# Kernel optimization log

Measured on AMD Instinct MI355X. Metric: run time of the kernel, lower is better.

Reference implementation:

```python
import jax, jax.numpy as jnp
import numpy as np

NEG = -9e15
ALPHA = 0.2  # LeakyReLU negative slope


def setup_inputs() -> dict:
    key = jax.random.key(0)
    k1, k2, k3, k4, k5, k6 = jax.random.split(key, 6)
    N, Fin, Fout = 8192, 512, 64
    x = jax.random.normal(k1, (N, Fin), dtype=jnp.float32)
    adj = jax.random.randint(k2, (N, N), 0, 2, dtype=jnp.int32)
    W = jax.random.normal(k3, (Fin, Fout), dtype=jnp.float32) * 0.05
    b = jax.random.normal(k4, (Fout,), dtype=jnp.float32) * 0.05
    a = jax.random.normal(k5, (2 * Fout,), dtype=jnp.float32) * 0.05
    a_b = jax.random.normal(k6, (), dtype=jnp.float32) * 0.05
    return {"x": x, "adj": adj, "W": W, "b": b, "a": a, "a_b": a_b}


def reference(x, adj, W, b, a, a_b):
    Fout = W.shape[1]
    h = x @ W + b  # [N, Fout]
    # attn([h_i, h_j]) decomposes: e[i,j] = h_i . a_src + h_j . a_dst + a_b
    # (avoids materializing the [N, N, 2F] concat tensor; same math)
    s_src = h @ a[:Fout]  # [N]
    s_dst = h @ a[Fout:]  # [N]
    energy = s_src[:, None] + s_dst[None, :] + a_b  # [N, N]
    energy = jnp.where(energy > 0, energy, ALPHA * energy)  # LeakyReLU
    masked = jnp.where(adj > 0, energy, NEG)
    attn = jax.nn.softmax(masked, axis=-1)  # dropout p=0 in eval
    h_prime = attn @ h  # [N, Fout]
    return jax.nn.elu(h_prime)  # concat=True path
```

## Files before the change

kernel.cpp:

```cpp
#include <hip/hip_runtime.h>
#include <hip/hip_bf16.h>

#define N_NODES 8192
#define FIN 512
#define FOUT 64
#define LRELU_ALPHA 0.2f

typedef __attribute__((ext_vector_type(8))) short short8;
typedef __attribute__((ext_vector_type(4))) float floatx4;

static __device__ __forceinline__ short f2bf_bits(float x) {
    union { __hip_bfloat16 b; short s; } u; u.b = __float2bfloat16(x); return u.s;
}

__global__ __launch_bounds__(256) void adj_bits(
    const int* __restrict__ adj, unsigned long long* __restrict__ bits)
{
    const int lane = threadIdx.x & 63;
    const int wid = blockIdx.x * 4 + (threadIdx.x >> 6);
    const size_t base = (size_t)wid * 128;
    const int* src = adj + base * 64 + lane;
    #pragma unroll 8
    for (int t = 0; t < 128; ++t) {
        int v = src[t * 64];
        unsigned long long m = __ballot(v > 0);
        if (lane == 0) bits[base + t] = m;
    }
}

#define GH_KT 128
__global__ __launch_bounds__(256) void gat_h(
    const float* __restrict__ x, const float* __restrict__ W,
    const float* __restrict__ bias, const float* __restrict__ a,
    const float* __restrict__ a_b,
    float* __restrict__ s_src, float* __restrict__ s_dst,
    unsigned short* __restrict__ hswz)
{
    __shared__ __align__(16) float xlds[2][16][GH_KT];

    const int lane = threadIdx.x & 63;
    const int wave = threadIdx.x >> 6;
    const int i0 = blockIdx.x * 16;
    const int r0 = i0 + wave * 4;

    auto stage = [&](int buf, int k0) {
        #pragma unroll
        for (int d = 0; d < 2; ++d) {
            const int row = wave * 4 + d * 2 + (lane >> 5);
            const float* g = x + (size_t)(i0 + row) * FIN + k0 + (lane & 31) * 4;
            __builtin_amdgcn_global_load_lds(
                (const __attribute__((address_space(1))) float*)g,
                (__attribute__((address_space(3))) float*)&xlds[buf][wave * 4 + d * 2][0],
                16, 0, 0);
        }
    };

    float acc0 = 0.f, acc1 = 0.f, acc2 = 0.f, acc3 = 0.f;

    stage(0, 0);
    for (int kt = 0; kt < FIN / GH_KT; ++kt) {
        asm volatile("s_waitcnt vmcnt(0)" ::: "memory");
        __builtin_amdgcn_sched_barrier(0);
        if (kt + 1 < FIN / GH_KT) stage((kt + 1) & 1, (kt + 1) * GH_KT);

        const float* xt = &xlds[kt & 1][wave * 4][0];
        const int k0 = kt * GH_KT;
        #pragma unroll 4
        for (int k4 = 0; k4 < GH_KT / 4; ++k4) {
            float w0 = W[(k0 + k4 * 4 + 0) * FOUT + lane];
            float w1 = W[(k0 + k4 * 4 + 1) * FOUT + lane];
            float w2 = W[(k0 + k4 * 4 + 2) * FOUT + lane];
            float w3 = W[(k0 + k4 * 4 + 3) * FOUT + lane];
            float4 xa = *reinterpret_cast<const float4*>(xt + 0 * GH_KT + k4 * 4);
            float4 xb = *reinterpret_cast<const float4*>(xt + 1 * GH_KT + k4 * 4);
            float4 xc = *reinterpret_cast<const float4*>(xt + 2 * GH_KT + k4 * 4);
            float4 xd = *reinterpret_cast<const float4*>(xt + 3 * GH_KT + k4 * 4);
            acc0 = fmaf(xa.w, w3, fmaf(xa.z, w2, fmaf(xa.y, w1, fmaf(xa.x, w0, acc0))));
            acc1 = fmaf(xb.w, w3, fmaf(xb.z, w2, fmaf(xb.y, w1, fmaf(xb.x, w0, acc1))));
            acc2 = fmaf(xc.w, w3, fmaf(xc.z, w2, fmaf(xc.y, w1, fmaf(xc.x, w0, acc2))));
            acc3 = fmaf(xd.w, w3, fmaf(xd.z, w2, fmaf(xd.y, w1, fmaf(xd.x, w0, acc3))));
        }
    }

    float bb = bias[lane];
    acc0 += bb; acc1 += bb; acc2 += bb; acc3 += bb;

    {
        const int ks = r0 >> 5;
        const int n = lane >> 4;
        const int lane_dst = (lane & 15) + (((r0 >> 3) & 3) << 4);
        const int e0 = r0 & 7;
        ushort4 pk;
        pk.x = (unsigned short)f2bf_bits(acc0);
        pk.y = (unsigned short)f2bf_bits(acc1);
        pk.z = (unsigned short)f2bf_bits(acc2);
        pk.w = (unsigned short)f2bf_bits(acc3);
        *reinterpret_cast<ushort4*>(
            hswz + (size_t)((ks * 4 + n) * 64 + lane_dst) * 8 + e0) = pk;
    }

    float asrc = a[lane], adst = a[FOUT + lane];
    float ab = a_b[0];
    float ss0 = acc0 * asrc, ss1 = acc1 * asrc, ss2 = acc2 * asrc, ss3 = acc3 * asrc;
    float sd0 = acc0 * adst, sd1 = acc1 * adst, sd2 = acc2 * adst, sd3 = acc3 * adst;
    #pragma unroll
    for (int m = 32; m >= 1; m >>= 1) {
        ss0 += __shfl_xor(ss0, m); ss1 += __shfl_xor(ss1, m);
        ss2 += __shfl_xor(ss2, m); ss3 += __shfl_xor(ss3, m);
        sd0 += __shfl_xor(sd0, m); sd1 += __shfl_xor(sd1, m);
        sd2 += __shfl_xor(sd2, m); sd3 += __shfl_xor(sd3, m);
    }
    if (lane == 0) {
        float4 vs = { ss0 + ab, ss1 + ab, ss2 + ab, ss3 + ab };
        float4 vd = { sd0, sd1, sd2, sd3 };
        *reinterpret_cast<float4*>(s_src + r0) = vs;
        *reinterpret_cast<float4*>(s_dst + r0) = vd;
    }
}

__global__ __launch_bounds__(512) void gat_attn(
    const unsigned int* __restrict__ bits,
    const float* __restrict__ s_src,
    const float* __restrict__ s_dst,
    const unsigned short* __restrict__ hswz,
    float* __restrict__ out)
{
    __shared__ __align__(16) char smem[33280];

    const int lane = threadIdx.x & 63;
    const int wave = threadIdx.x >> 6;
    const int i0 = blockIdx.x * 16;
    const int r = lane & 15;
    const int g = lane >> 4;

    #pragma unroll
    for (int i = 0; i < 2; ++i) {
        const int c = threadIdx.x + i * 512;
        const int row = c >> 6, col = c & 63;
        uint4 v = *reinterpret_cast<const uint4*>(bits + (size_t)(i0 + row) * 256 + col * 4);
        *reinterpret_cast<uint4*>(smem + row * 1040 + col * 16) = v;
    }
    __syncthreads();

    const float ssrc = s_src[i0 + r];
    floatx4 acc[4] = { {0.f,0.f,0.f,0.f},{0.f,0.f,0.f,0.f},
                       {0.f,0.f,0.f,0.f},{0.f,0.f,0.f,0.f} };
    float denom = 0.f;

    const char* bl = smem + r * 1040 + (wave << 3);

    for (int s = 0; s < 16; ++s) {
        uint2 bw = *reinterpret_cast<const uint2*>(bl + s * 64);
        #pragma unroll
        for (int kk = 0; kk < 2; ++kk) {
            const unsigned byte = ((kk ? bw.y : bw.x) >> (g * 8)) & 0xffu;
            const int jb = s * 512 + wave * 64 + kk * 32 + g * 8;
            float4 S0 = *reinterpret_cast<const float4*>(s_dst + jb);
            float4 S1 = *reinterpret_cast<const float4*>(s_dst + jb + 4);
            float e0 = ssrc + S0.x, e1 = ssrc + S0.y, e2 = ssrc + S0.z, e3 = ssrc + S0.w;
            float e4 = ssrc + S1.x, e5 = ssrc + S1.y, e6 = ssrc + S1.z, e7 = ssrc + S1.w;
            e0 = fmaxf(e0, LRELU_ALPHA * e0); e1 = fmaxf(e1, LRELU_ALPHA * e1);
            e2 = fmaxf(e2, LRELU_ALPHA * e2); e3 = fmaxf(e3, LRELU_ALPHA * e3);
            e4 = fmaxf(e4, LRELU_ALPHA * e4); e5 = fmaxf(e5, LRELU_ALPHA * e5);
            e6 = fmaxf(e6, LRELU_ALPHA * e6); e7 = fmaxf(e7, LRELU_ALPHA * e7);
            float p0 = (byte & 1u)   ? __expf(e0) : 0.f;
            float p1 = (byte & 2u)   ? __expf(e1) : 0.f;
            float p2 = (byte & 4u)   ? __expf(e2) : 0.f;
            float p3 = (byte & 8u)   ? __expf(e3) : 0.f;
            float p4 = (byte & 16u)  ? __expf(e4) : 0.f;
            float p5 = (byte & 32u)  ? __expf(e5) : 0.f;
            float p6 = (byte & 64u)  ? __expf(e6) : 0.f;
            float p7 = (byte & 128u) ? __expf(e7) : 0.f;
            denom += ((p0 + p1) + (p2 + p3)) + ((p4 + p5) + (p6 + p7));
            short8 af;
            af[0] = f2bf_bits(p0); af[1] = f2bf_bits(p1);
            af[2] = f2bf_bits(p2); af[3] = f2bf_bits(p3);
            af[4] = f2bf_bits(p4); af[5] = f2bf_bits(p5);
            af[6] = f2bf_bits(p6); af[7] = f2bf_bits(p7);
            const int ks = s * 16 + wave * 2 + kk;
            #pragma unroll
            for (int n = 0; n < 4; ++n) {
                short8 bf = *reinterpret_cast<const short8*>(
                    hswz + (size_t)((ks * 4 + n) * 64 + lane) * 8);
                acc[n] = __builtin_amdgcn_mfma_f32_16x16x32_bf16(af, bf, acc[n], 0, 0, 0);
            }
        }
    }

    denom += __shfl_xor(denom, 16);
    denom += __shfl_xor(denom, 32);

    __syncthreads();
    floatx4* redbuf = (floatx4*)smem;
    float* dred = (float*)(smem + 32768);
    #pragma unroll
    for (int n = 0; n < 4; ++n) redbuf[(wave * 4 + n) * 64 + lane] = acc[n];
    if (lane < 16) dred[wave * 16 + lane] = denom;
    __syncthreads();

    if (wave < 4) {
        floatx4 facc = redbuf[wave * 64 + lane];
        #pragma unroll
        for (int v = 1; v < 8; ++v) facc += redbuf[(v * 4 + wave) * 64 + lane];
        #pragma unroll
        for (int e = 0; e < 4; ++e) {
            const int r2 = (lane >> 4) * 4 + e;
            float dn = 0.f;
            #pragma unroll
            for (int v = 0; v < 8; ++v) dn += dred[v * 16 + r2];
            float val = facc[e] / dn;
            val = val > 0.f ? val : (__expf(val) - 1.f);
            out[(size_t)(i0 + r2) * FOUT + wave * 16 + (lane & 15)] = val;
        }
    }
}

extern "C" void kernel_launch(void* const* d_in, const int* in_sizes, int n_in,
                              void* d_out, int out_size, void* d_ws, size_t ws_size,
                              hipStream_t stream) {
    const float* x   = (const float*)d_in[0];
    const int*   adj = (const int*)d_in[1];
    const float* W   = (const float*)d_in[2];
    const float* b   = (const float*)d_in[3];
    const float* a   = (const float*)d_in[4];
    const float* a_b = (const float*)d_in[5];
    float* out = (float*)d_out;

    char* ws = (char*)d_ws;
    float* s_src = (float*)ws;
    float* s_dst = (float*)(ws + 32 * 1024);
    unsigned short* hswz = (unsigned short*)(ws + 64 * 1024);
    unsigned long long* bitsW = (unsigned long long*)(ws + 64 * 1024 + 1024 * 1024);
    const unsigned int* bitsR = (const unsigned int*)bitsW;

    hipLaunchKernelGGL(adj_bits, dim3(N_NODES / 4), dim3(256), 0, stream, adj, bitsW);
    hipLaunchKernelGGL(gat_h, dim3(N_NODES / 16), dim3(256), 0, stream,
                       x, W, b, a, a_b, s_src, s_dst, hswz);
    hipLaunchKernelGGL(gat_attn, dim3(N_NODES / 16), dim3(512), 0, stream,
                       bitsR, s_src, s_dst, hswz, out);
}
```

Before: 164.2 us.

## Fuse prep kernels and factor exp of LeakyReLU into precomputed products

Merges the adjacency bit-packing kernel and the h/score kernel into one launch, using a block-index split. In the attention loop, exp(leakyrelu(si+sj)) is rewritten as a product of precomputed per-node exponentials, picking exp(si)exp(sj) or exp(0.2si)exp(0.2sj) depending on whether the product exceeds 1. This removes the per-edge exp and LeakyReLU math in favour of multiplies and selects. It also packs the bf16 conversions with v_cvt_pk_bf16_f32, at the cost of doubling the s_dst read bandwidth and some risk of exp overflow or underflow for large scores.

```diff
diff --git a/kernel.cpp b/kernel.cpp
--- a/kernel.cpp
+++ b/kernel.cpp
@@ -4,7 +4,6 @@
 #define N_NODES 8192
 #define FIN 512
 #define FOUT 64
-#define LRELU_ALPHA 0.2f
 
 typedef __attribute__((ext_vector_type(8))) short short8;
 typedef __attribute__((ext_vector_type(4))) float floatx4;
@@ -13,50 +12,49 @@
     union { __hip_bfloat16 b; short s; } u; u.b = __float2bfloat16(x); return u.s;
 }
 
-__global__ __launch_bounds__(256) void adj_bits(
-    const int* __restrict__ adj, unsigned long long* __restrict__ bits)
-{
-    const int lane = threadIdx.x & 63;
-    const int wid = blockIdx.x * 4 + (threadIdx.x >> 6);
-    const size_t base = (size_t)wid * 128;
-    const int* src = adj + base * 64 + lane;
-    #pragma unroll 8
-    for (int t = 0; t < 128; ++t) {
-        int v = src[t * 64];
-        unsigned long long m = __ballot(v > 0);
-        if (lane == 0) bits[base + t] = m;
-    }
-}
-
 #define GH_KT 128
-__global__ __launch_bounds__(256) void gat_h(
+__global__ __launch_bounds__(256) void prep(
+    const int* __restrict__ adj, unsigned long long* __restrict__ bits,
     const float* __restrict__ x, const float* __restrict__ W,
     const float* __restrict__ bias, const float* __restrict__ a,
     const float* __restrict__ a_b,
-    float* __restrict__ s_src, float* __restrict__ s_dst,
+    float2* __restrict__ EFi, float2* __restrict__ EFd,
     unsigned short* __restrict__ hswz)
 {
     __shared__ __align__(16) float xlds[2][16][GH_KT];
 
     const int lane = threadIdx.x & 63;
     const int wave = threadIdx.x >> 6;
+
+    if (blockIdx.x >= 512) {
+        const int wid = (blockIdx.x - 512) * 4 + wave;
+        const size_t base = (size_t)wid * 128;
+        const int* src = adj + base * 64 + lane;
+        #pragma unroll 8
+        for (int t = 0; t < 128; ++t) {
+            int v = src[t * 64];
+            unsigned long long m = __ballot(v > 0);
+            if (lane == 0) bits[base + t] = m;
+        }
+        return;
+    }
+
     const int i0 = blockIdx.x * 16;
     const int r0 = i0 + wave * 4;
 
     auto stage = [&](int buf, int k0) {
         #pragma unroll
         for (int d = 0; d < 2; ++d) {
-            const int row = wave * 4 + d * 2 + (lane >> 5);
-            const float* g = x + (size_t)(i0 + row) * FIN + k0 + (lane & 31) * 4;
+            const float* gp = x + (size_t)(i0 + wave * 4 + d * 2 + (lane >> 5)) * FIN
+                            + k0 + (lane & 31) * 4;
             __builtin_amdgcn_global_load_lds(
-                (const __attribute__((address_space(1))) float*)g,
+                (const __attribute__((address_space(1))) float*)gp,
                 (__attribute__((address_space(3))) float*)&xlds[buf][wave * 4 + d * 2][0],
                 16, 0, 0);
         }
     };
 
     float acc0 = 0.f, acc1 = 0.f, acc2 = 0.f, acc3 = 0.f;
-
     stage(0, 0);
     for (int kt = 0; kt < FIN / GH_KT; ++kt) {
         asm volatile("s_waitcnt vmcnt(0)" ::: "memory");
@@ -111,21 +109,27 @@
         sd2 += __shfl_xor(sd2, m); sd3 += __shfl_xor(sd3, m);
     }
     if (lane == 0) {
-        float4 vs = { ss0 + ab, ss1 + ab, ss2 + ab, ss3 + ab };
-        float4 vd = { sd0, sd1, sd2, sd3 };
-        *reinterpret_cast<float4*>(s_src + r0) = vs;
-        *reinterpret_cast<float4*>(s_dst + r0) = vd;
+        float si0 = ss0 + ab, si1 = ss1 + ab, si2 = ss2 + ab, si3 = ss3 + ab;
+        EFi[r0 + 0] = make_float2(__expf(si0), __expf(0.2f * si0));
+        EFi[r0 + 1] = make_float2(__expf(si1), __expf(0.2f * si1));
+        EFi[r0 + 2] = make_float2(__expf(si2), __expf(0.2f * si2));
+        EFi[r0 + 3] = make_float2(__expf(si3), __expf(0.2f * si3));
+        EFd[r0 + 0] = make_float2(__expf(sd0), __expf(0.2f * sd0));
+        EFd[r0 + 1] = make_float2(__expf(sd1), __expf(0.2f * sd1));
+        EFd[r0 + 2] = make_float2(__expf(sd2), __expf(0.2f * sd2));
+        EFd[r0 + 3] = make_float2(__expf(sd3), __expf(0.2f * sd3));
     }
 }
 
 __global__ __launch_bounds__(512) void gat_attn(
     const unsigned int* __restrict__ bits,
-    const float* __restrict__ s_src,
-    const float* __restrict__ s_dst,
+    const float2* __restrict__ EFi,
+    const float2* __restrict__ EFd,
     const unsigned short* __restrict__ hswz,
     float* __restrict__ out)
 {
-    __shared__ __align__(16) char smem[33280];
+    __shared__ __align__(16) char bsmem[16640];
+    __shared__ __align__(16) char rsmem[33280];
 
     const int lane = threadIdx.x & 63;
     const int wave = threadIdx.x >> 6;
@@ -138,45 +142,53 @@
         const int c = threadIdx.x + i * 512;
         const int row = c >> 6, col = c & 63;
         uint4 v = *reinterpret_cast<const uint4*>(bits + (size_t)(i0 + row) * 256 + col * 4);
-        *reinterpret_cast<uint4*>(smem + row * 1040 + col * 16) = v;
+        *reinterpret_cast<uint4*>(bsmem + row * 1040 + col * 16) = v;
     }
     __syncthreads();
 
-    const float ssrc = s_src[i0 + r];
+    const float2 efi = EFi[i0 + r];
+    const float Es = efi.x, Fs = efi.y;
+    const char* bl = bsmem + r * 1040 + (wave << 3);
+
     floatx4 acc[4] = { {0.f,0.f,0.f,0.f},{0.f,0.f,0.f,0.f},
                        {0.f,0.f,0.f,0.f},{0.f,0.f,0.f,0.f} };
     float denom = 0.f;
 
-    const char* bl = smem + r * 1040 + (wave << 3);
-
     for (int s = 0; s < 16; ++s) {
         uint2 bw = *reinterpret_cast<const uint2*>(bl + s * 64);
         #pragma unroll
         for (int kk = 0; kk < 2; ++kk) {
             const unsigned byte = ((kk ? bw.y : bw.x) >> (g * 8)) & 0xffu;
             const int jb = s * 512 + wave * 64 + kk * 32 + g * 8;
-            float4 S0 = *reinterpret_cast<const float4*>(s_dst + jb);
-            float4 S1 = *reinterpret_cast<const float4*>(s_dst + jb + 4);
-            float e0 = ssrc + S0.x, e1 = ssrc + S0.y, e2 = ssrc + S0.z, e3 = ssrc + S0.w;
-            float e4 = ssrc + S1.x, e5 = ssrc + S1.y, e6 = ssrc + S1.z, e7 = ssrc + S1.w;
-            e0 = fmaxf(e0, LRELU_ALPHA * e0); e1 = fmaxf(e1, LRELU_ALPHA * e1);
-            e2 = fmaxf(e2, LRELU_ALPHA * e2); e3 = fmaxf(e3, LRELU_ALPHA * e3);
-            e4 = fmaxf(e4, LRELU_ALPHA * e4); e5 = fmaxf(e5, LRELU_ALPHA * e5);
-            e6 = fmaxf(e6, LRELU_ALPHA * e6); e7 = fmaxf(e7, LRELU_ALPHA * e7);
-            float p0 = (byte & 1u)   ? __expf(e0) : 0.f;
-            float p1 = (byte & 2u)   ? __expf(e1) : 0.f;
-            float p2 = (byte & 4u)   ? __expf(e2) : 0.f;
-            float p3 = (byte & 8u)   ? __expf(e3) : 0.f;
-            float p4 = (byte & 16u)  ? __expf(e4) : 0.f;
-            float p5 = (byte & 32u)  ? __expf(e5) : 0.f;
-            float p6 = (byte & 64u)  ? __expf(e6) : 0.f;
-            float p7 = (byte & 128u) ? __expf(e7) : 0.f;
+            const float4* ef = reinterpret_cast<const float4*>(EFd + jb);
+            float4 q0 = ef[0];
+            float4 q1 = ef[1];
+            float4 q2 = ef[2];
+            float4 q3 = ef[3];
+            float m0 = Es * q0.x, f0 = Fs * q0.y;
+            float m1 = Es * q0.z, f1 = Fs * q0.w;
+            float m2 = Es * q1.x, f2 = Fs * q1.y;
+            float m3 = Es * q1.z, f3 = Fs * q1.w;
+            float m4 = Es * q2.x, f4 = Fs * q2.y;
+            float m5 = Es * q2.z, f5 = Fs * q2.w;
+            float m6 = Es * q3.x, f6 = Fs * q3.y;
+            float m7 = Es * q3.z, f7 = Fs * q3.w;
+            float p0 = m0 > 1.0f ? m0 : f0;  p0 = (byte & 1u)   ? p0 : 0.f;
+            float p1 = m1 > 1.0f ? m1 : f1;  p1 = (byte & 2u)   ? p1 : 0.f;
+            float p2 = m2 > 1.0f ? m2 : f2;  p2 = (byte & 4u)   ? p2 : 0.f;
+            float p3 = m3 > 1.0f ? m3 : f3;  p3 = (byte & 8u)   ? p3 : 0.f;
+            float p4 = m4 > 1.0f ? m4 : f4;  p4 = (byte & 16u)  ? p4 : 0.f;
+            float p5 = m5 > 1.0f ? m5 : f5;  p5 = (byte & 32u)  ? p5 : 0.f;
+            float p6 = m6 > 1.0f ? m6 : f6;  p6 = (byte & 64u)  ? p6 : 0.f;
+            float p7 = m7 > 1.0f ? m7 : f7;  p7 = (byte & 128u) ? p7 : 0.f;
             denom += ((p0 + p1) + (p2 + p3)) + ((p4 + p5) + (p6 + p7));
-            short8 af;
-            af[0] = f2bf_bits(p0); af[1] = f2bf_bits(p1);
-            af[2] = f2bf_bits(p2); af[3] = f2bf_bits(p3);
-            af[4] = f2bf_bits(p4); af[5] = f2bf_bits(p5);
-            af[6] = f2bf_bits(p6); af[7] = f2bf_bits(p7);
+            unsigned r01, r23, r45, r67;
+            asm("v_cvt_pk_bf16_f32 %0, %1, %2" : "=v"(r01) : "v"(p0), "v"(p1));
+            asm("v_cvt_pk_bf16_f32 %0, %1, %2" : "=v"(r23) : "v"(p2), "v"(p3));
+            asm("v_cvt_pk_bf16_f32 %0, %1, %2" : "=v"(r45) : "v"(p4), "v"(p5));
+            asm("v_cvt_pk_bf16_f32 %0, %1, %2" : "=v"(r67) : "v"(p6), "v"(p7));
+            int4 ai = { (int)r01, (int)r23, (int)r45, (int)r67 };
+            short8 af = *reinterpret_cast<short8*>(&ai);
             const int ks = s * 16 + wave * 2 + kk;
             #pragma unroll
             for (int n = 0; n < 4; ++n) {
@@ -191,8 +203,8 @@
     denom += __shfl_xor(denom, 32);
 
     __syncthreads();
-    floatx4* redbuf = (floatx4*)smem;
-    float* dred = (float*)(smem + 32768);
+    floatx4* redbuf = (floatx4*)rsmem;
+    float* dred = (float*)(rsmem + 32768);
     #pragma unroll
     for (int n = 0; n < 4; ++n) redbuf[(wave * 4 + n) * 64 + lane] = acc[n];
     if (lane < 16) dred[wave * 16 + lane] = denom;
@@ -227,15 +239,14 @@
     float* out = (float*)d_out;
 
     char* ws = (char*)d_ws;
-    float* s_src = (float*)ws;
-    float* s_dst = (float*)(ws + 32 * 1024);
-    unsigned short* hswz = (unsigned short*)(ws + 64 * 1024);
-    unsigned long long* bitsW = (unsigned long long*)(ws + 64 * 1024 + 1024 * 1024);
+    float2* EFi = (float2*)ws;
+    float2* EFd = (float2*)(ws + 64 * 1024);
+    unsigned short* hswz = (unsigned short*)(ws + 128 * 1024);
+    unsigned long long* bitsW = (unsigned long long*)(ws + 128 * 1024 + 1024 * 1024);
     const unsigned int* bitsR = (const unsigned int*)bitsW;
 
-    hipLaunchKernelGGL(adj_bits, dim3(N_NODES / 4), dim3(256), 0, stream, adj, bitsW);
-    hipLaunchKernelGGL(gat_h, dim3(N_NODES / 16), dim3(256), 0, stream,
-                       x, W, b, a, a_b, s_src, s_dst, hswz);
+    hipLaunchKernelGGL(prep, dim3(512 + N_NODES / 4), dim3(256), 0, stream,
+                       adj, bitsW, x, W, b, a, a_b, EFi, EFd, hswz);
     hipLaunchKernelGGL(gat_attn, dim3(N_NODES / 16), dim3(512), 0, stream,
-                       bitsR, s_src, s_dst, hswz, out);
-}
+                       bitsR, EFi, EFd, hswz, out);
+}
```

New measurement: 212.0 us. 1.29x slower.
